# Kernel optimization log

Measured on AMD Instinct MI355X. Metric: run time of the kernel, lower is better.

Reference implementation:

```python
import jax, jax.numpy as jnp
import numpy as np

B, T, IN, H, L = 64, 1024, 512, 1024, 2
ZO = 0.1  # zoneout prob; eval-mode blend factor


def setup_inputs() -> dict:
    key = jax.random.key(0)
    ks = jax.random.split(key, 9)
    s = 1.0 / np.sqrt(H)  # torch GRUCell uniform init bound

    def w(k, shape):
        return jax.random.uniform(k, shape, jnp.float32, -s, s)

    return dict(
        x=jax.random.normal(ks[0], (B, T, IN), jnp.float32),
        h0=jnp.zeros((L, B, H), jnp.float32),
        w_ih_0=w(ks[1], (3 * H, IN)),
        w_hh_0=w(ks[2], (3 * H, H)),
        b_ih_0=w(ks[3], (3 * H,)),
        b_hh_0=w(ks[4], (3 * H,)),
        w_ih_1=w(ks[5], (3 * H, H)),
        w_hh_1=w(ks[6], (3 * H, H)),
        b_ih_1=w(ks[7], (3 * H,)),
        b_hh_1=w(ks[8], (3 * H,)),
    )


def _gru_cell(inp, h, w_ih, w_hh, b_ih, b_hh):
    # PyTorch GRUCell gate math; gi/gh: [B, 3H]
    gi = inp @ w_ih.T + b_ih
    gh = h @ w_hh.T + b_hh
    i_r, i_z, i_n = jnp.split(gi, 3, axis=-1)
    h_r, h_z, h_n = jnp.split(gh, 3, axis=-1)
    r = jax.nn.sigmoid(i_r + h_r)
    z = jax.nn.sigmoid(i_z + h_z)
    n = jnp.tanh(i_n + r * h_n)
    return (1.0 - z) * n + z * h


def reference(x, h0, w_ih_0, w_hh_0, b_ih_0, b_hh_0, w_ih_1, w_hh_1, b_ih_1, b_hh_1):
    params = [
        (w_ih_0, w_hh_0, b_ih_0, b_hh_0),
        (w_ih_1, w_hh_1, b_ih_1, b_hh_1),
    ]

    def step(h, x_t):  # h: [L,B,H], x_t: [B,IN]
        inp = x_t
        new_hs = []
        for i in range(L):
            nh = _gru_cell(inp, h[i], *params[i])
            # eval-mode zoneout: deterministic blend with prob ZO
            nh = ZO * h[i] + (1.0 - ZO) * nh
            new_hs.append(nh)
            inp = nh  # layer_drop inactive in eval
        return jnp.stack(new_hs), inp

    h_n, outs = jax.lax.scan(step, h0, jnp.swapaxes(x, 0, 1))  # outs: [T,B,H]
    return jnp.swapaxes(outs, 0, 1), h_n
```

## Files before the change

kernel.cpp:

```cpp
#include <hip/hip_runtime.h>


#define Tn 1024
#define Hn 1024
#define INn 512

typedef short s8v __attribute__((ext_vector_type(8)));
typedef float f4v __attribute__((ext_vector_type(4)));
typedef unsigned short us4v __attribute__((ext_vector_type(4)));
typedef unsigned long long ull;

#define WS_XB  0u
#define WS_H0R 67108864u
#define WS_H1R 134217728u
#define WS_MB  167772160u

__device__ __forceinline__ unsigned short f2bf(float f) {
  unsigned int u = __float_as_uint(f);
  u += 0x7fffu + ((u >> 16) & 1u);
  return (unsigned short)(u >> 16);
}

__device__ __forceinline__ s8v pack8(const float* p) {
  float4 a = *(const float4*)p;
  float4 b = *(const float4*)(p + 4);
  s8v r;
  r[0] = (short)f2bf(a.x); r[1] = (short)f2bf(a.y);
  r[2] = (short)f2bf(a.z); r[3] = (short)f2bf(a.w);
  r[4] = (short)f2bf(b.x); r[5] = (short)f2bf(b.y);
  r[6] = (short)f2bf(b.z); r[7] = (short)f2bf(b.w);
  return r;
}

__device__ __forceinline__ void st8c(unsigned short* p, us4v v) {
  union { us4v v; ull u; } c; c.v = v;
  __hip_atomic_store((ull*)p, c.u, __ATOMIC_RELAXED, __HIP_MEMORY_SCOPE_AGENT);
}

__device__ __forceinline__ void stnt16(float* p, f4v v) {
  asm volatile("global_store_dwordx4 %0, %1, off nt" :: "v"(p), "v"(v) : "memory");
}

__device__ __forceinline__ void issue4c(s8v* f, const unsigned short* src,
                                        int kt, int w, int rl, int kg) {
#pragma unroll
  for (int m = 0; m < 4; ++m) {
    const unsigned short* p = src + (size_t)(w * 16 + kt * 2 + (kg >> 1)) * 1024
                              + (m * 16 + rl) * 16 + (kg & 1) * 8;
    asm volatile("global_load_dwordx4 %0, %1, off"
                 : "=v"(f[m]) : "v"(p) : "memory");
  }
}

template<int N> __device__ __forceinline__ void vmwait() {
  asm volatile("s_waitcnt vmcnt(%0)" :: "i"(N) : "memory");
  __builtin_amdgcn_sched_barrier(0);
}

__device__ __forceinline__ void mfma3(f4v (*acc)[4], s8v w0, s8v w1, s8v w2,
                                      const s8v f[4], const int gl) {
#pragma unroll
  for (int m = 0; m < 4; ++m) {
    acc[m][0]  = __builtin_amdgcn_mfma_f32_16x16x32_bf16(w0, f[m], acc[m][0], 0, 0, 0);
    acc[m][1]  = __builtin_amdgcn_mfma_f32_16x16x32_bf16(w1, f[m], acc[m][1], 0, 0, 0);
    acc[m][gl] = __builtin_amdgcn_mfma_f32_16x16x32_bf16(w2, f[m], acc[m][gl], 0, 0, 0);
  }
}

template<int GL>
__device__ __forceinline__ void stream_gemm_deep(f4v (*acc)[4], const s8v (*wgt)[8],
    const unsigned short* src, int w, int rl, int kg) {
  s8v f[6][4];
#pragma unroll
  for (int kt = 0; kt < 6; ++kt) issue4c(f[kt], src, kt, w, rl, kg);
  vmwait<20>(); mfma3(acc, wgt[0][0], wgt[1][0], wgt[2][0], f[0], GL);
  issue4c(f[0], src, 6, w, rl, kg);
  vmwait<20>(); mfma3(acc, wgt[0][1], wgt[1][1], wgt[2][1], f[1], GL);
  issue4c(f[1], src, 7, w, rl, kg);
  vmwait<20>(); mfma3(acc, wgt[0][2], wgt[1][2], wgt[2][2], f[2], GL);
  vmwait<16>(); mfma3(acc, wgt[0][3], wgt[1][3], wgt[2][3], f[3], GL);
  vmwait<12>(); mfma3(acc, wgt[0][4], wgt[1][4], wgt[2][4], f[4], GL);
  vmwait<8>();  mfma3(acc, wgt[0][5], wgt[1][5], wgt[2][5], f[5], GL);
  vmwait<4>();  mfma3(acc, wgt[0][6], wgt[1][6], wgt[2][6], f[0], GL);
  vmwait<0>();  mfma3(acc, wgt[0][7], wgt[1][7], wgt[2][7], f[1], GL);
}

__global__ void cvt_bf16_kernel(const float* __restrict__ src,
                                unsigned short* __restrict__ dst, int n4) {
  int i = blockIdx.x * blockDim.x + threadIdx.x;
  int st = gridDim.x * blockDim.x;
  for (; i < n4; i += st) {
    const float4 v = *(const float4*)(src + 4 * (size_t)i);
    us4v o;
    o[0] = f2bf(v.x); o[1] = f2bf(v.y); o[2] = f2bf(v.z); o[3] = f2bf(v.w);
    *(us4v*)(dst + 4 * (size_t)i) = o;
  }
}

__global__ void init_all(const float* __restrict__ h0in, char* __restrict__ ws) {
  int i = blockIdx.x * blockDim.x + threadIdx.x;
  unsigned short* h0r = (unsigned short*)(ws + WS_H0R);
  unsigned short* h1r = (unsigned short*)(ws + WS_H1R);
  int* MB = (int*)(ws + WS_MB);
  if (i < 65536) {
    int b = i >> 10, h = i & 1023;
    int off = (h >> 4) * 1024 + b * 16 + (h & 15);
    h0r[511 * 65536 + off] = f2bf(h0in[i]);
    h1r[255 * 65536 + off] = f2bf(h0in[65536 + i]);
  }
  if (i < 32768) MB[i] = 0;
}

__device__ __forceinline__ void mb_wait(const int* MB, int r1, int t1,
                                        int r2, int t2, int lane) {
  const int* p1 = MB + (r1 * 64 + lane);
  const int* p2 = MB + (r2 * 64 + lane);
  int tries = 0;
  for (;;) {
    int v1 = __hip_atomic_load(p1, __ATOMIC_RELAXED, __HIP_MEMORY_SCOPE_AGENT);
    int v2 = __hip_atomic_load(p2, __ATOMIC_RELAXED, __HIP_MEMORY_SCOPE_AGENT);
    if (__all(v1 >= t1 && v2 >= t2)) return;
    __builtin_amdgcn_s_sleep(1);
    if (++tries > (1 << 22)) return;
  }
}

__global__ __launch_bounds__(256)
__attribute__((amdgpu_waves_per_eu(1, 1)))
void gru_persist(
    const float* __restrict__ h0in,
    const float* __restrict__ wih0, const float* __restrict__ whh0,
    const float* __restrict__ bih0, const float* __restrict__ bhh0,
    const float* __restrict__ wih1, const float* __restrict__ whh1,
    const float* __restrict__ bih1, const float* __restrict__ bhh1,
    float* __restrict__ out, char* __restrict__ ws)
{
  const unsigned short* xb = (const unsigned short*)(ws + WS_XB);
  unsigned short* h0r = (unsigned short*)(ws + WS_H0R);
  unsigned short* h1r = (unsigned short*)(ws + WS_H1R);
  int* MB = (int*)(ws + WS_MB);

  const int blk = blockIdx.x;
  const int tid = threadIdx.x;

  if (blk >= 128) {
    const int c = blk & 63;
    float a0 = 1.0f + (float)tid * 1e-6f, a1 = a0 + 0.25f;
    float a2 = a0 + 0.5f, a3 = a0 + 0.75f;
    const float mm = 0.99999988f, cc = 1e-7f;
    int run = 1;
    for (int it = 0; it < (1 << 17) && run; ++it) {
#pragma unroll
      for (int u = 0; u < 256; ++u) {
        a0 = __builtin_fmaf(a0, mm, cc); a1 = __builtin_fmaf(a1, mm, cc);
        a2 = __builtin_fmaf(a2, mm, cc); a3 = __builtin_fmaf(a3, mm, cc);
      }
      if ((it & 15) == 0) {
        int v = __hip_atomic_load(MB + (((2 * 64) + c) * 64 + (tid & 63)),
                                  __ATOMIC_RELAXED, __HIP_MEMORY_SCOPE_AGENT);
        if (__all(v >= Tn)) run = 0;
      }
    }
    asm volatile("" :: "v"(a0), "v"(a1), "v"(a2), "v"(a3));
    return;
  }

  const bool isA = blk < 64;
  const int jt = blk & 63, jj = jt * 16;
  const int w = tid >> 6;
  const int lane = tid & 63;
  const int rl = lane & 15, kg = lane >> 4;

  __shared__ float cmb[4][4][64][20];

  const int b = w * 16 + rl;
  const int j0 = jj + kg * 4;

  const float* Wi = isA ? wih0 : wih1;
  const float* Wh = isA ? whh0 : whh1;
  const float* bi = isA ? bih0 : bih1;
  const float* bh = isA ? bhh0 : bhh1;
  s8v wx[3][8], wh_[3][8];
#pragma unroll
  for (int g = 0; g < 3; ++g) {
    if (isA) {
#pragma unroll
      for (int kt = 0; kt < 4; ++kt)
        wx[g][kt] = pack8(Wi + (size_t)(g * 1024 + jj + rl) * INn + w * 128 + kt * 32 + kg * 8);
    } else {
#pragma unroll
      for (int kt = 0; kt < 8; ++kt)
        wx[g][kt] = pack8(Wi + (size_t)(g * 1024 + jj + rl) * Hn + w * 256 + kt * 32 + kg * 8);
    }
#pragma unroll
    for (int kt = 0; kt < 8; ++kt)
      wh_[g][kt] = pack8(Wh + (size_t)(g * 1024 + jj + rl) * Hn + w * 256 + kt * 32 + kg * 8);
  }
  const f4v bir = *(const f4v*)(bi + j0),        bhr = *(const f4v*)(bh + j0);
  const f4v biz = *(const f4v*)(bi + 1024 + j0), bhz = *(const f4v*)(bh + 1024 + j0);
  const f4v bin = *(const f4v*)(bi + 2048 + j0), bhn = *(const f4v*)(bh + 2048 + j0);

  f4v hv = *(const f4v*)(h0in + (isA ? 0u : 65536u) + (size_t)b * Hn + j0);

  for (int s = 0; s < Tn; ++s) {
    s8v bx[4][4];
    if (isA) {
#pragma unroll
      for (int m = 0; m < 4; ++m)
#pragma unroll
        for (int kt = 0; kt < 4; ++kt)
          bx[m][kt] = *(const s8v*)(xb + ((size_t)(m * 16 + rl) * Tn + s) * INn + w * 128 + kt * 32 + kg * 8);
    }
    if (w == 0) {
      if (isA) mb_wait(MB, 0 * 64 + jt, s,     3 * 64 + jt, s - 255, lane);
      else     mb_wait(MB, 1 * 64 + jt, s + 1, 2 * 64 + jt, s,       lane);
    }
    __syncthreads();
    vmwait<0>();

    f4v acc[4][4];
#pragma unroll
    for (int m = 0; m < 4; ++m)
#pragma unroll
      for (int g = 0; g < 4; ++g) acc[m][g] = (f4v){0.f, 0.f, 0.f, 0.f};

    const unsigned short* hsrc = isA ? (h0r + (size_t)((s - 1) & 511) * 65536)
                                     : (h1r + (size_t)((s - 1) & 255) * 65536);
    const unsigned short* asrc = h0r + (size_t)(s & 511) * 65536;

    if (isA) {
#pragma unroll
      for (int kt = 0; kt < 4; ++kt) {
        s8v f4[4] = { bx[0][kt], bx[1][kt], bx[2][kt], bx[3][kt] };
        mfma3(acc, wx[0][kt], wx[1][kt], wx[2][kt], f4, 2);
      }
      stream_gemm_deep<3>(acc, wh_, hsrc, w, rl, kg);
    } else {
      stream_gemm_deep<2>(acc, wx, asrc, w, rl, kg);
      stream_gemm_deep<3>(acc, wh_, hsrc, w, rl, kg);
    }

#pragma unroll
    for (int d = 0; d < 4; ++d) if (d != w)
#pragma unroll
      for (int g = 0; g < 4; ++g) *(f4v*)&cmb[d][w][lane][g * 4] = acc[d][g];
    __syncthreads();
    f4v hsum[4];
#pragma unroll
    for (int g = 0; g < 4; ++g) {
      hsum[g] = acc[w][g];
#pragma unroll
      for (int src = 0; src < 4; ++src) if (src != w) hsum[g] += *(f4v*)&cmb[w][src][lane][g * 4];
    }

    us4v hb4;
#pragma unroll
    for (int rr = 0; rr < 4; ++rr) {
      float hp = hv[rr];
      float rg = 1.f / (1.f + __expf(-(hsum[0][rr] + bir[rr] + bhr[rr])));
      float zg = 1.f / (1.f + __expf(-(hsum[1][rr] + biz[rr] + bhz[rr])));
      float narg = hsum[2][rr] + bin[rr] + rg * (hsum[3][rr] + bhn[rr]);
      float e2 = __expf(2.f * narg);
      float ng = 1.f - 2.f / (e2 + 1.f);
      float nv = (1.f - zg) * ng + zg * hp;
      hv[rr] = 0.1f * hp + 0.9f * nv;
    }
    hb4[0] = f2bf(hv[0]); hb4[1] = f2bf(hv[1]); hb4[2] = f2bf(hv[2]); hb4[3] = f2bf(hv[3]);

    if (isA) {
      st8c(h0r + (size_t)(s & 511) * 65536 + jt * 1024 + b * 16 + kg * 4, hb4);
      if (s == Tn - 1)
        stnt16(out + 67108864u + (size_t)b * Hn + j0, hv);
      vmwait<0>();
    } else {
      st8c(h1r + (size_t)(s & 255) * 65536 + jt * 1024 + b * 16 + kg * 4, hb4);
      stnt16(out + ((size_t)b * Tn + s) * Hn + j0, hv);
      if (s == Tn - 1) {
        stnt16(out + 67108864u + 65536u + (size_t)b * Hn + j0, hv);
        vmwait<0>();
      } else {
        vmwait<1>();
      }
    }
    __syncthreads();
    if (tid < 64) {
      const int g1 = isA ? 0 : 2, g2 = isA ? 1 : 3;
      __hip_atomic_store(MB + ((g1 * 64 + tid) * 64 + jt), s + 1,
                         __ATOMIC_RELAXED, __HIP_MEMORY_SCOPE_AGENT);
      __hip_atomic_store(MB + ((g2 * 64 + tid) * 64 + jt), s + 1,
                         __ATOMIC_RELAXED, __HIP_MEMORY_SCOPE_AGENT);
    }
  }
}

extern "C" void kernel_launch(void* const* d_in, const int* in_sizes, int n_in,
                              void* d_out, int out_size, void* d_ws, size_t ws_size,
                              hipStream_t stream) {
  (void)in_sizes; (void)n_in; (void)out_size; (void)ws_size;
  const float* x    = (const float*)d_in[0];
  const float* h0in = (const float*)d_in[1];
  const float* wih0 = (const float*)d_in[2];
  const float* whh0 = (const float*)d_in[3];
  const float* bih0 = (const float*)d_in[4];
  const float* bhh0 = (const float*)d_in[5];
  const float* wih1 = (const float*)d_in[6];
  const float* whh1 = (const float*)d_in[7];
  const float* bih1 = (const float*)d_in[8];
  const float* bhh1 = (const float*)d_in[9];
  float* out = (float*)d_out;
  char* ws = (char*)d_ws;

  cvt_bf16_kernel<<<2048, 256, 0, stream>>>(x, (unsigned short*)(ws + WS_XB), 33554432 / 4);
  init_all<<<528, 256, 0, stream>>>(h0in, ws);
  gru_persist<<<dim3(256), dim3(256), 0, stream>>>(
      h0in, wih0, whh0, bih0, bhh0, wih1, whh1, bih1, bhh1, out, ws);
}
```

Baseline: 7.817 ms.

## Split layer-1 blocks into input-GEMM and recurrent-GEMM warp roles with separate waits

Layer-1 blocks now give two warps the input projection (h0 of the current step) and two warps the recurrent projection (h1 of the previous step). Each warp covers half of K with 16 k-tiles in a deeper streaming loop, and each role waits only on its own mailbox dependency. Before, every warp streamed both GEMMs in sequence after a single combined wait. The aim is to start the input-side GEMM before the recurrent dependency is satisfied, shortening the critical path per step. Each warp now holds 48 weight fragments, which raises register pressure. The barrier structure also changes, because each warp does its own mb_wait without the earlier syncthreads.

Measured after the change: 7.673 ms (median of 2 runs). About the same (-1.8%).

```diff
diff --git a/kernel.cpp b/kernel.cpp
--- a/kernel.cpp
+++ b/kernel.cpp
@@ -42,10 +42,10 @@
 }
 
 __device__ __forceinline__ void issue4c(s8v* f, const unsigned short* src,
-                                        int kt, int w, int rl, int kg) {
+                                        int base, int kt, int rl, int kg) {
 #pragma unroll
   for (int m = 0; m < 4; ++m) {
-    const unsigned short* p = src + (size_t)(w * 16 + kt * 2 + (kg >> 1)) * 1024
+    const unsigned short* p = src + (size_t)(base + kt * 2 + (kg >> 1)) * 1024
                               + (m * 16 + rl) * 16 + (kg & 1) * 8;
     asm volatile("global_load_dwordx4 %0, %1, off"
                  : "=v"(f[m]) : "v"(p) : "memory");
@@ -68,21 +68,45 @@
 }
 
 template<int GL>
-__device__ __forceinline__ void stream_gemm_deep(f4v (*acc)[4], const s8v (*wgt)[8],
-    const unsigned short* src, int w, int rl, int kg) {
+__device__ __forceinline__ void stream8(f4v (*acc)[4], const s8v (*wgt)[8],
+    const unsigned short* src, int base, int rl, int kg) {
   s8v f[6][4];
 #pragma unroll
-  for (int kt = 0; kt < 6; ++kt) issue4c(f[kt], src, kt, w, rl, kg);
+  for (int kt = 0; kt < 6; ++kt) issue4c(f[kt], src, base, kt, rl, kg);
   vmwait<20>(); mfma3(acc, wgt[0][0], wgt[1][0], wgt[2][0], f[0], GL);
-  issue4c(f[0], src, 6, w, rl, kg);
+  issue4c(f[0], src, base, 6, rl, kg);
   vmwait<20>(); mfma3(acc, wgt[0][1], wgt[1][1], wgt[2][1], f[1], GL);
-  issue4c(f[1], src, 7, w, rl, kg);
+  issue4c(f[1], src, base, 7, rl, kg);
   vmwait<20>(); mfma3(acc, wgt[0][2], wgt[1][2], wgt[2][2], f[2], GL);
   vmwait<16>(); mfma3(acc, wgt[0][3], wgt[1][3], wgt[2][3], f[3], GL);
   vmwait<12>(); mfma3(acc, wgt[0][4], wgt[1][4], wgt[2][4], f[4], GL);
   vmwait<8>();  mfma3(acc, wgt[0][5], wgt[1][5], wgt[2][5], f[5], GL);
   vmwait<4>();  mfma3(acc, wgt[0][6], wgt[1][6], wgt[2][6], f[0], GL);
   vmwait<0>();  mfma3(acc, wgt[0][7], wgt[1][7], wgt[2][7], f[1], GL);
+}
+
+template<int GL>
+__device__ __forceinline__ void stream16(f4v (*acc)[4], const s8v (*wgt)[16],
+    const unsigned short* src, int base, int rl, int kg) {
+  s8v f[6][4];
+#pragma unroll
+  for (int kt = 0; kt < 6; ++kt) issue4c(f[kt], src, base, kt, rl, kg);
+  vmwait<20>(); mfma3(acc, wgt[0][0],  wgt[1][0],  wgt[2][0],  f[0], GL); issue4c(f[0], src, base, 6,  rl, kg);
+  vmwait<20>(); mfma3(acc, wgt[0][1],  wgt[1][1],  wgt[2][1],  f[1], GL); issue4c(f[1], src, base, 7,  rl, kg);
+  vmwait<20>(); mfma3(acc, wgt[0][2],  wgt[1][2],  wgt[2][2],  f[2], GL); issue4c(f[2], src, base, 8,  rl, kg);
+  vmwait<20>(); mfma3(acc, wgt[0][3],  wgt[1][3],  wgt[2][3],  f[3], GL); issue4c(f[3], src, base, 9,  rl, kg);
+  vmwait<20>(); mfma3(acc, wgt[0][4],  wgt[1][4],  wgt[2][4],  f[4], GL); issue4c(f[4], src, base, 10, rl, kg);
+  vmwait<20>(); mfma3(acc, wgt[0][5],  wgt[1][5],  wgt[2][5],  f[5], GL); issue4c(f[5], src, base, 11, rl, kg);
+  vmwait<20>(); mfma3(acc, wgt[0][6],  wgt[1][6],  wgt[2][6],  f[0], GL); issue4c(f[0], src, base, 12, rl, kg);
+  vmwait<20>(); mfma3(acc, wgt[0][7],  wgt[1][7],  wgt[2][7],  f[1], GL); issue4c(f[1], src, base, 13, rl, kg);
+  vmwait<20>(); mfma3(acc, wgt[0][8],  wgt[1][8],  wgt[2][8],  f[2], GL); issue4c(f[2], src, base, 14, rl, kg);
+  vmwait<20>(); mfma3(acc, wgt[0][9],  wgt[1][9],  wgt[2][9],  f[3], GL); issue4c(f[3], src, base, 15, rl, kg);
+  vmwait<20>(); mfma3(acc, wgt[0][10], wgt[1][10], wgt[2][10], f[4], GL);
+  vmwait<16>(); mfma3(acc, wgt[0][11], wgt[1][11], wgt[2][11], f[5], GL);
+  vmwait<12>(); mfma3(acc, wgt[0][12], wgt[1][12], wgt[2][12], f[0], GL);
+  vmwait<8>();  mfma3(acc, wgt[0][13], wgt[1][13], wgt[2][13], f[1], GL);
+  vmwait<4>();  mfma3(acc, wgt[0][14], wgt[1][14], wgt[2][14], f[2], GL);
+  vmwait<0>();  mfma3(acc, wgt[0][15], wgt[1][15], wgt[2][15], f[3], GL);
 }
 
 __global__ void cvt_bf16_kernel(const float* __restrict__ src,
@@ -176,103 +200,148 @@
   const int b = w * 16 + rl;
   const int j0 = jj + kg * 4;
 
-  const float* Wi = isA ? wih0 : wih1;
-  const float* Wh = isA ? whh0 : whh1;
   const float* bi = isA ? bih0 : bih1;
   const float* bh = isA ? bhh0 : bhh1;
-  s8v wx[3][8], wh_[3][8];
-#pragma unroll
-  for (int g = 0; g < 3; ++g) {
-    if (isA) {
-#pragma unroll
-      for (int kt = 0; kt < 4; ++kt)
-        wx[g][kt] = pack8(Wi + (size_t)(g * 1024 + jj + rl) * INn + w * 128 + kt * 32 + kg * 8);
-    } else {
-#pragma unroll
-      for (int kt = 0; kt < 8; ++kt)
-        wx[g][kt] = pack8(Wi + (size_t)(g * 1024 + jj + rl) * Hn + w * 256 + kt * 32 + kg * 8);
-    }
-#pragma unroll
-    for (int kt = 0; kt < 8; ++kt)
-      wh_[g][kt] = pack8(Wh + (size_t)(g * 1024 + jj + rl) * Hn + w * 256 + kt * 32 + kg * 8);
-  }
   const f4v bir = *(const f4v*)(bi + j0),        bhr = *(const f4v*)(bh + j0);
   const f4v biz = *(const f4v*)(bi + 1024 + j0), bhz = *(const f4v*)(bh + 1024 + j0);
   const f4v bin = *(const f4v*)(bi + 2048 + j0), bhn = *(const f4v*)(bh + 2048 + j0);
 
   f4v hv = *(const f4v*)(h0in + (isA ? 0u : 65536u) + (size_t)b * Hn + j0);
 
-  for (int s = 0; s < Tn; ++s) {
-    s8v bx[4][4];
-    if (isA) {
+  if (isA) {
+    s8v wx[3][4], wh_[3][8];
+#pragma unroll
+    for (int g = 0; g < 3; ++g) {
+#pragma unroll
+      for (int kt = 0; kt < 4; ++kt)
+        wx[g][kt] = pack8(wih0 + (size_t)(g * 1024 + jj + rl) * INn + w * 128 + kt * 32 + kg * 8);
+#pragma unroll
+      for (int kt = 0; kt < 8; ++kt)
+        wh_[g][kt] = pack8(whh0 + (size_t)(g * 1024 + jj + rl) * Hn + w * 256 + kt * 32 + kg * 8);
+    }
+
+    for (int s = 0; s < Tn; ++s) {
+      s8v bx[4][4];
 #pragma unroll
       for (int m = 0; m < 4; ++m)
 #pragma unroll
         for (int kt = 0; kt < 4; ++kt)
           bx[m][kt] = *(const s8v*)(xb + ((size_t)(m * 16 + rl) * Tn + s) * INn + w * 128 + kt * 32 + kg * 8);
-    }
-    if (w == 0) {
-      if (isA) mb_wait(MB, 0 * 64 + jt, s,     3 * 64 + jt, s - 255, lane);
-      else     mb_wait(MB, 1 * 64 + jt, s + 1, 2 * 64 + jt, s,       lane);
-    }
-    __syncthreads();
-    vmwait<0>();
-
-    f4v acc[4][4];
-#pragma unroll
-    for (int m = 0; m < 4; ++m)
-#pragma unroll
-      for (int g = 0; g < 4; ++g) acc[m][g] = (f4v){0.f, 0.f, 0.f, 0.f};
-
-    const unsigned short* hsrc = isA ? (h0r + (size_t)((s - 1) & 511) * 65536)
-                                     : (h1r + (size_t)((s - 1) & 255) * 65536);
-    const unsigned short* asrc = h0r + (size_t)(s & 511) * 65536;
-
-    if (isA) {
+      if (w == 0) mb_wait(MB, 0 * 64 + jt, s, 3 * 64 + jt, s - 255, lane);
+      __syncthreads();
+      vmwait<0>();
+
+      f4v acc[4][4];
+#pragma unroll
+      for (int m = 0; m < 4; ++m)
+#pragma unroll
+        for (int g = 0; g < 4; ++g) acc[m][g] = (f4v){0.f, 0.f, 0.f, 0.f};
+
+      const unsigned short* hsrc = h0r + (size_t)((s - 1) & 511) * 65536;
 #pragma unroll
       for (int kt = 0; kt < 4; ++kt) {
         s8v f4[4] = { bx[0][kt], bx[1][kt], bx[2][kt], bx[3][kt] };
         mfma3(acc, wx[0][kt], wx[1][kt], wx[2][kt], f4, 2);
       }
-      stream_gemm_deep<3>(acc, wh_, hsrc, w, rl, kg);
-    } else {
-      stream_gemm_deep<2>(acc, wx, asrc, w, rl, kg);
-      stream_gemm_deep<3>(acc, wh_, hsrc, w, rl, kg);
-    }
-
-#pragma unroll
-    for (int d = 0; d < 4; ++d) if (d != w)
-#pragma unroll
-      for (int g = 0; g < 4; ++g) *(f4v*)&cmb[d][w][lane][g * 4] = acc[d][g];
-    __syncthreads();
-    f4v hsum[4];
-#pragma unroll
-    for (int g = 0; g < 4; ++g) {
-      hsum[g] = acc[w][g];
-#pragma unroll
-      for (int src = 0; src < 4; ++src) if (src != w) hsum[g] += *(f4v*)&cmb[w][src][lane][g * 4];
-    }
-
-    us4v hb4;
-#pragma unroll
-    for (int rr = 0; rr < 4; ++rr) {
-      float hp = hv[rr];
-      float rg = 1.f / (1.f + __expf(-(hsum[0][rr] + bir[rr] + bhr[rr])));
-      float zg = 1.f / (1.f + __expf(-(hsum[1][rr] + biz[rr] + bhz[rr])));
-      float narg = hsum[2][rr] + bin[rr] + rg * (hsum[3][rr] + bhn[rr]);
-      float e2 = __expf(2.f * narg);
-      float ng = 1.f - 2.f / (e2 + 1.f);
-      float nv = (1.f - zg) * ng + zg * hp;
-      hv[rr] = 0.1f * hp + 0.9f * nv;
-    }
-    hb4[0] = f2bf(hv[0]); hb4[1] = f2bf(hv[1]); hb4[2] = f2bf(hv[2]); hb4[3] = f2bf(hv[3]);
-
-    if (isA) {
+      stream8<3>(acc, wh_, hsrc, w * 16, rl, kg);
+
+#pragma unroll
+      for (int d = 0; d < 4; ++d) if (d != w)
+#pragma unroll
+        for (int g = 0; g < 4; ++g) *(f4v*)&cmb[d][w][lane][g * 4] = acc[d][g];
+      __syncthreads();
+      f4v hsum[4];
+#pragma unroll
+      for (int g = 0; g < 4; ++g) {
+        hsum[g] = acc[w][g];
+#pragma unroll
+        for (int src = 0; src < 4; ++src) if (src != w) hsum[g] += *(f4v*)&cmb[w][src][lane][g * 4];
+      }
+
+      us4v hb4;
+#pragma unroll
+      for (int rr = 0; rr < 4; ++rr) {
+        float hp = hv[rr];
+        float rg = 1.f / (1.f + __expf(-(hsum[0][rr] + bir[rr] + bhr[rr])));
+        float zg = 1.f / (1.f + __expf(-(hsum[1][rr] + biz[rr] + bhz[rr])));
+        float narg = hsum[2][rr] + bin[rr] + rg * (hsum[3][rr] + bhn[rr]);
+        float e2 = __expf(2.f * narg);
+        float ng = 1.f - 2.f / (e2 + 1.f);
+        float nv = (1.f - zg) * ng + zg * hp;
+        hv[rr] = 0.1f * hp + 0.9f * nv;
+      }
+      hb4[0] = f2bf(hv[0]); hb4[1] = f2bf(hv[1]); hb4[2] = f2bf(hv[2]); hb4[3] = f2bf(hv[3]);
+
       st8c(h0r + (size_t)(s & 511) * 65536 + jt * 1024 + b * 16 + kg * 4, hb4);
       if (s == Tn - 1)
         stnt16(out + 67108864u + (size_t)b * Hn + j0, hv);
       vmwait<0>();
-    } else {
+      __syncthreads();
+      if (tid < 64) {
+        __hip_atomic_store(MB + ((0 * 64 + tid) * 64 + jt), s + 1,
+                           __ATOMIC_RELAXED, __HIP_MEMORY_SCOPE_AGENT);
+        __hip_atomic_store(MB + ((1 * 64 + tid) * 64 + jt), s + 1,
+                           __ATOMIC_RELAXED, __HIP_MEMORY_SCOPE_AGENT);
+      }
+    }
+  } else {
+    const int role = w >> 1;
+    const int half = w & 1;
+    const float* Wsrc = role ? whh1 : wih1;
+    s8v wgt[3][16];
+#pragma unroll
+    for (int g = 0; g < 3; ++g)
+#pragma unroll
+      for (int kt = 0; kt < 16; ++kt)
+        wgt[g][kt] = pack8(Wsrc + (size_t)(g * 1024 + jj + rl) * Hn + half * 512 + kt * 32 + kg * 8);
+
+    for (int s = 0; s < Tn; ++s) {
+      f4v acc[4][4];
+#pragma unroll
+      for (int m = 0; m < 4; ++m)
+#pragma unroll
+        for (int g = 0; g < 4; ++g) acc[m][g] = (f4v){0.f, 0.f, 0.f, 0.f};
+
+      const unsigned short* hsrc = h1r + (size_t)((s - 1) & 255) * 65536;
+      const unsigned short* asrc = h0r + (size_t)(s & 511) * 65536;
+
+      if (role == 0) {
+        mb_wait(MB, 1 * 64 + jt, s + 1, 1 * 64 + jt, s + 1, lane);
+        vmwait<0>();
+        stream16<2>(acc, wgt, asrc, half * 32, rl, kg);
+      } else {
+        mb_wait(MB, 2 * 64 + jt, s, 2 * 64 + jt, s, lane);
+        vmwait<0>();
+        stream16<3>(acc, wgt, hsrc, half * 32, rl, kg);
+      }
+
+#pragma unroll
+      for (int d = 0; d < 4; ++d) if (d != w)
+#pragma unroll
+        for (int g = 0; g < 4; ++g) *(f4v*)&cmb[d][w][lane][g * 4] = acc[d][g];
+      __syncthreads();
+      f4v hsum[4];
+#pragma unroll
+      for (int g = 0; g < 4; ++g) {
+        hsum[g] = acc[w][g];
+#pragma unroll
+        for (int src = 0; src < 4; ++src) if (src != w) hsum[g] += *(f4v*)&cmb[w][src][lane][g * 4];
+      }
+
+      us4v hb4;
+#pragma unroll
+      for (int rr = 0; rr < 4; ++rr) {
+        float hp = hv[rr];
+        float rg = 1.f / (1.f + __expf(-(hsum[0][rr] + bir[rr] + bhr[rr])));
+        float zg = 1.f / (1.f + __expf(-(hsum[1][rr] + biz[rr] + bhz[rr])));
+        float narg = hsum[2][rr] + bin[rr] + rg * (hsum[3][rr] + bhn[rr]);
+        float e2 = __expf(2.f * narg);
+        float ng = 1.f - 2.f / (e2 + 1.f);
+        float nv = (1.f - zg) * ng + zg * hp;
+        hv[rr] = 0.1f * hp + 0.9f * nv;
+      }
+      hb4[0] = f2bf(hv[0]); hb4[1] = f2bf(hv[1]); hb4[2] = f2bf(hv[2]); hb4[3] = f2bf(hv[3]);
+
       st8c(h1r + (size_t)(s & 255) * 65536 + jt * 1024 + b * 16 + kg * 4, hb4);
       stnt16(out + ((size_t)b * Tn + s) * Hn + j0, hv);
       if (s == Tn - 1) {
@@ -281,14 +350,13 @@
       } else {
         vmwait<1>();
       }
-    }
-    __syncthreads();
-    if (tid < 64) {
-      const int g1 = isA ? 0 : 2, g2 = isA ? 1 : 3;
-      __hip_atomic_store(MB + ((g1 * 64 + tid) * 64 + jt), s + 1,
-                         __ATOMIC_RELAXED, __HIP_MEMORY_SCOPE_AGENT);
-      __hip_atomic_store(MB + ((g2 * 64 + tid) * 64 + jt), s + 1,
-                         __ATOMIC_RELAXED, __HIP_MEMORY_SCOPE_AGENT);
+      __syncthreads();
+      if (tid < 64) {
+        __hip_atomic_store(MB + ((2 * 64 + tid) * 64 + jt), s + 1,
+                           __ATOMIC_RELAXED, __HIP_MEMORY_SCOPE_AGENT);
+        __hip_atomic_store(MB + ((3 * 64 + tid) * 64 + jt), s + 1,
+                           __ATOMIC_RELAXED, __HIP_MEMORY_SCOPE_AGENT);
+      }
     }
   }
 }
```
